# Kernel tuning notes

Hardware: AMD Instinct MI355X
Metric: run time of the kernel (lower is better)

The kernel has to match this reference:

```python
import jax, jax.numpy as jnp
import numpy as np

D_MODEL = 1024
NUM_EXP = 64
EPS = 1e-9
B, L = 16, 2048


def setup_inputs() -> dict:
    key = jax.random.key(0)
    ks = jax.random.split(key, 12)
    s = 1.0 / np.sqrt(D_MODEL)
    inp = {
        "x": jax.random.normal(ks[0], (B, L, D_MODEL), dtype=jnp.float32),
        "n_indexes": jax.random.randint(ks[1], (B, NUM_EXP), 0, NUM_EXP),
        "mask": jax.random.randint(ks[2], (B, 1, L), 0, 2).astype(jnp.int32),
        "q_emb": jax.random.normal(ks[3], (NUM_EXP, D_MODEL), dtype=jnp.float32),
        "b_emb": jax.random.normal(ks[4], (NUM_EXP, D_MODEL), dtype=jnp.float32),
        "Wk": jax.random.normal(ks[5], (D_MODEL, D_MODEL), dtype=jnp.float32) * s,
        "bk": jnp.zeros((D_MODEL,), jnp.float32),
        "Wa": jax.random.normal(ks[6], (D_MODEL, D_MODEL), dtype=jnp.float32) * s,
        "ba": jnp.zeros((D_MODEL,), jnp.float32),
        "Wb": jax.random.normal(ks[7], (D_MODEL, D_MODEL), dtype=jnp.float32) * s,
        "bb": jnp.zeros((D_MODEL,), jnp.float32),
        "Ws": jax.random.normal(ks[8], (D_MODEL, D_MODEL), dtype=jnp.float32) * s,
        "bs": jnp.zeros((D_MODEL,), jnp.float32),
    }
    return inp


def reference(x, n_indexes, mask, q_emb, b_emb, Wk, bk, Wa, ba, Wb, bb, Ws, bs):
    # Dropout layers act as identity (eval mode).
    query_exp = q_emb[n_indexes]          # [B, E, D]
    bias_exp = b_emb[n_indexes]           # [B, E, D]
    x_key = x @ Wk.T + bk                 # [B, L, D]
    z = jnp.einsum('bed,bld->bel', query_exp, x_key) / np.sqrt(D_MODEL)  # [B, E, L]

    maskf = (mask != 0).astype(z.dtype)   # broadcast [B,1,L]
    class_a_fw = jax.nn.relu(z) * maskf
    class_b_fw = jax.nn.relu(-z) * maskf
    class_a_fw = class_a_fw / (class_a_fw.sum(-1, keepdims=True) + EPS)
    class_b_fw = class_b_fw / (class_b_fw.sum(-1, keepdims=True) + EPS)

    class_a = jnp.einsum('bel,bld->bed', class_a_fw, x @ Wa.T + ba) + bias_exp
    class_b = jnp.einsum('bel,bld->bed', class_b_fw, x @ Wb.T + bb) + bias_exp

    zt = jnp.swapaxes(z, -2, -1)          # [B, L, E]  (unmasked, as in source)
    class_a_bw = jax.nn.relu(zt)
    class_b_bw = jax.nn.relu(-zt)
    class_a_bw = class_a_bw / (class_a_bw.sum(-1, keepdims=True) + EPS)
    class_b_bw = class_b_bw / (class_b_bw.sum(-1, keepdims=True) + EPS)

    class_a = jnp.einsum('ble,bed->bld', class_a_bw, class_a)  # [B, L, D]
    class_b = jnp.einsum('ble,bed->bld', class_b_bw, class_b)

    selector = jax.nn.sigmoid(x @ Ws.T + bs)
    return selector * class_a + (1.0 - selector) * class_b
```

## Files before the change

kernel.cpp:

```cpp
#include <hip/hip_runtime.h>
#include <math.h>

#define D_MODEL 1024
#define NUM_EXP 64
#define B_SZ 16
#define L_SZ 2048

using bf16x8  = __attribute__((ext_vector_type(8))) __bf16;
using floatx4 = __attribute__((ext_vector_type(4))) float;
using ushort8 = __attribute__((ext_vector_type(8))) unsigned short;
using ushort4v = __attribute__((ext_vector_type(4))) unsigned short;

__device__ __forceinline__ unsigned short f2bf(float f) {
    union { float f; unsigned u; } x; x.f = f;
    unsigned r = (x.u + 0x7fffu + ((x.u >> 16) & 1u)) >> 16;
    return (unsigned short)r;
}
__device__ __forceinline__ float bf2f(unsigned short h) {
    union { unsigned u; float f; } x; x.u = ((unsigned)h) << 16;
    return x.f;
}

#define GLD16(gp, lp) __builtin_amdgcn_global_load_lds( \
    (const __attribute__((address_space(1))) unsigned int*)(gp), \
    (__attribute__((address_space(3))) unsigned int*)(lp), 16, 0, 0)

__global__ void k_convx(const float* __restrict__ in, unsigned short* __restrict__ outN,
                        unsigned short* __restrict__ outT)
{
    __shared__ unsigned short T[64][65];
    const int b = blockIdx.z;
    const int l0 = blockIdx.y * 64, c0 = blockIdx.x * 64;
    const int t = threadIdx.x;
    const int tr = t >> 4, tc = (t & 15) * 4;
    const float* src = in + ((long)b * L_SZ + l0) * D_MODEL + c0;
    unsigned short* dN = outN + ((long)b * L_SZ + l0) * D_MODEL + c0;
    #pragma unroll
    for (int i = 0; i < 4; i++) {
        int r = tr + i * 16;
        float4 v = *(const float4*)(src + (long)r * D_MODEL + tc);
        ushort4v u; u[0]=f2bf(v.x); u[1]=f2bf(v.y); u[2]=f2bf(v.z); u[3]=f2bf(v.w);
        *(ushort4v*)(dN + (long)r * D_MODEL + tc) = u;
        T[r][tc+0]=u[0]; T[r][tc+1]=u[1]; T[r][tc+2]=u[2]; T[r][tc+3]=u[3];
    }
    __syncthreads();
    unsigned short* dT = outT + ((long)b * D_MODEL + c0) * L_SZ + l0;
    #pragma unroll
    for (int i = 0; i < 4; i++) {
        int c = tr + i * 16;
        ushort4v u;
        u[0]=T[tc+0][c]; u[1]=T[tc+1][c]; u[2]=T[tc+2][c]; u[3]=T[tc+3][c];
        *(ushort4v*)(dT + (long)c * L_SZ + tc) = u;
    }
}

__global__ void k_prep(const float* __restrict__ Wk,
                       const float* __restrict__ Wa, const float* __restrict__ Wb,
                       const float* __restrict__ Ws,
                       const int* __restrict__ idx, const float* __restrict__ q_emb,
                       const float* __restrict__ b_emb, const float* __restrict__ bk,
                       unsigned short* __restrict__ wkT,
                       unsigned short* __restrict__ oa, unsigned short* __restrict__ ob,
                       unsigned short* __restrict__ oc,
                       unsigned short* __restrict__ qexp, float* __restrict__ bias_exp,
                       float* __restrict__ qbk)
{
    __shared__ unsigned short T[64][65];
    __shared__ float red[4];
    const int blk = blockIdx.x;
    const int t = threadIdx.x;
    if (blk < 256) {
        const int r0 = (blk >> 4) * 64, c0 = (blk & 15) * 64;
        const int tr = t >> 4, tc = (t & 15) * 4;
        const float* src = Wk + (long)r0 * D_MODEL + c0;
        #pragma unroll
        for (int i = 0; i < 4; i++) {
            int r = tr + i * 16;
            float4 v = *(const float4*)(src + (long)r * D_MODEL + tc);
            T[r][tc+0]=f2bf(v.x); T[r][tc+1]=f2bf(v.y); T[r][tc+2]=f2bf(v.z); T[r][tc+3]=f2bf(v.w);
        }
        __syncthreads();
        unsigned short* dT = wkT + ((long)c0) * D_MODEL + r0;
        #pragma unroll
        for (int i = 0; i < 4; i++) {
            int c = tr + i * 16;
            ushort4v u;
            u[0]=T[tc+0][c]; u[1]=T[tc+1][c]; u[2]=T[tc+2][c]; u[3]=T[tc+3][c];
            *(ushort4v*)(dT + (long)c * D_MODEL + tc) = u;
        }
    } else if (blk < 256 + 1536) {
        long i = ((long)(blk - 256) * 256 + t) * 8;
        int which = (int)(i >> 20);
        long off = i & ((1L << 20) - 1);
        const float* src = which == 0 ? Wa : which == 1 ? Wb : Ws;
        unsigned short* dst = which == 0 ? oa : which == 1 ? ob : oc;
        float4 v0 = *(const float4*)(src + off);
        float4 v1 = *(const float4*)(src + off + 4);
        ushort8 r;
        r[0]=f2bf(v0.x); r[1]=f2bf(v0.y); r[2]=f2bf(v0.z); r[3]=f2bf(v0.w);
        r[4]=f2bf(v1.x); r[5]=f2bf(v1.y); r[6]=f2bf(v1.z); r[7]=f2bf(v1.w);
        *(ushort8*)(dst + off) = r;
    } else {
        const int be = blk - 1792;
        const int row = idx[be];
        const float* qs = q_emb + (long)row * D_MODEL;
        const float* bsrc = b_emb + (long)row * D_MODEL;
        float4 q4 = *(const float4*)(qs + t * 4);
        float4 k4 = *(const float4*)(bk + t * 4);
        float4 b4 = *(const float4*)(bsrc + t * 4);
        ushort4v r; r[0]=f2bf(q4.x); r[1]=f2bf(q4.y); r[2]=f2bf(q4.z); r[3]=f2bf(q4.w);
        *(ushort4v*)(qexp + (long)be * D_MODEL + t * 4) = r;
        *(float4*)(bias_exp + (long)be * D_MODEL + t * 4) = b4;
        float p = q4.x*k4.x + q4.y*k4.y + q4.z*k4.z + q4.w*k4.w;
        #pragma unroll
        for (int o = 32; o > 0; o >>= 1) p += __shfl_down(p, o);
        if ((t & 63) == 0) red[t >> 6] = p;
        __syncthreads();
        if (t == 0) qbk[be] = red[0] + red[1] + red[2] + red[3];
    }
}

__launch_bounds__(256)
__global__ void k_gemm_bt(const unsigned short* __restrict__ A,
                          const unsigned short* __restrict__ Bm,
                          const float* __restrict__ rowbias,
                          void* __restrict__ Cout,
                          int M, int N, int K, float scale, int flags,
                          long sA, long sB, long sC)
{
    __shared__ __align__(16) unsigned short As[64 * 32];
    __shared__ __align__(16) unsigned short Bs[64 * 32];
    const int bz = blockIdx.z;
    const unsigned short* Ab = A + (long)bz * sA;
    const unsigned short* Bb = Bm + (long)bz * sB;
    const int tid = threadIdx.x;
    const int wave = tid >> 6, lane = tid & 63;
    const int m0 = blockIdx.y * 64, n0 = blockIdx.x * 64;
    const int lrow = tid >> 2, lk = (tid & 3) * 8;
    const int q = lane >> 4, mr = lane & 15;

    floatx4 acc[4];
    floatx4 z4 = {0.f, 0.f, 0.f, 0.f};
    #pragma unroll
    for (int j = 0; j < 4; j++) acc[j] = z4;

    const unsigned short* Aptr = Ab + (long)(m0 + lrow) * K + lk;
    const unsigned short* Bptr = Bb + (long)(n0 + lrow) * K + lk;

    for (int k0 = 0; k0 < K; k0 += 32) {
        __syncthreads();
        *(ushort8*)&As[lrow * 32 + lk] = *(const ushort8*)(Aptr + k0);
        *(ushort8*)&Bs[lrow * 32 + lk] = *(const ushort8*)(Bptr + k0);
        __syncthreads();
        bf16x8 af = *(const bf16x8*)&As[(wave * 16 + mr) * 32 + q * 8];
        #pragma unroll
        for (int j = 0; j < 4; j++) {
            bf16x8 bfr = *(const bf16x8*)&Bs[(j * 16 + mr) * 32 + q * 8];
            acc[j] = __builtin_amdgcn_mfma_f32_16x16x32_bf16(af, bfr, acc[j], 0, 0, 0);
        }
    }
    #pragma unroll
    for (int j = 0; j < 4; j++) {
        int gn = n0 + j * 16 + mr;
        #pragma unroll
        for (int r = 0; r < 4; r++) {
            int gm = m0 + wave * 16 + q * 4 + r;
            float v = acc[j][r];
            if (rowbias) v += rowbias[(long)bz * M + gm];
            v *= scale;
            long cidx = (long)bz * sC + (long)gm * N + gn;
            if (flags & 1) ((unsigned short*)Cout)[cidx] = f2bf(v);
            else           ((float*)Cout)[cidx] = v;
        }
    }
}

__launch_bounds__(512)
__global__ void k_gemm_fw2(const unsigned short* __restrict__ A1,
                           const unsigned short* __restrict__ A2,
                           const unsigned short* __restrict__ Bt,
                           unsigned short* __restrict__ C1,
                           unsigned short* __restrict__ C2)
{
    __shared__ __align__(16) unsigned short As1[2][64 * 32];
    __shared__ __align__(16) unsigned short As2[2][64 * 32];
    __shared__ __align__(16) unsigned short Bs[2][64 * 32];
    __shared__ float Red[2][64][65];
    const int bz = blockIdx.z;
    const int n0 = blockIdx.x * 64;
    const int tid = threadIdx.x;
    const int grp = tid >> 8;
    const int gtid = tid & 255;
    const int wave = gtid >> 6, lane = tid & 63;
    const int lrow = gtid >> 2, lk = (gtid & 3) * 8;
    const int q = lane >> 4, mr = lane & 15;
    const int kb = grp * (L_SZ / 2);

    const unsigned short* a1p = A1 + ((long)bz * NUM_EXP + lrow) * L_SZ + kb + lk;
    const unsigned short* a2p = A2 + ((long)bz * NUM_EXP + lrow) * L_SZ + kb + lk;
    const unsigned short* bp  = Bt + ((long)bz * D_MODEL + n0 + lrow) * L_SZ + kb + lk;

    floatx4 acc1[4], acc2[4];
    floatx4 z4 = {0.f, 0.f, 0.f, 0.f};
    #pragma unroll
    for (int j = 0; j < 4; j++) { acc1[j] = z4; acc2[j] = z4; }

    for (int k0 = 0; k0 < L_SZ / 2; k0 += 32) {
        __syncthreads();
        *(ushort8*)&As1[grp][lrow * 32 + lk] = *(const ushort8*)(a1p + k0);
        *(ushort8*)&As2[grp][lrow * 32 + lk] = *(const ushort8*)(a2p + k0);
        *(ushort8*)&Bs[grp][lrow * 32 + lk]  = *(const ushort8*)(bp + k0);
        __syncthreads();
        bf16x8 f1 = *(const bf16x8*)&As1[grp][(wave * 16 + mr) * 32 + q * 8];
        bf16x8 f2 = *(const bf16x8*)&As2[grp][(wave * 16 + mr) * 32 + q * 8];
        #pragma unroll
        for (int j = 0; j < 4; j++) {
            bf16x8 bb = *(const bf16x8*)&Bs[grp][(j * 16 + mr) * 32 + q * 8];
            acc1[j] = __builtin_amdgcn_mfma_f32_16x16x32_bf16(f1, bb, acc1[j], 0, 0, 0);
            acc2[j] = __builtin_amdgcn_mfma_f32_16x16x32_bf16(f2, bb, acc2[j], 0, 0, 0);
        }
    }
    __syncthreads();
    if (grp == 1) {
        #pragma unroll
        for (int j = 0; j < 4; j++)
            #pragma unroll
            for (int r = 0; r < 4; r++) {
                int gm = wave * 16 + q * 4 + r;
                Red[0][gm][j * 16 + mr] = acc1[j][r];
                Red[1][gm][j * 16 + mr] = acc2[j][r];
            }
    }
    __syncthreads();
    if (grp == 0) {
        #pragma unroll
        for (int j = 0; j < 4; j++) {
            int gn = n0 + j * 16 + mr;
            #pragma unroll
            for (int r = 0; r < 4; r++) {
                int gm = wave * 16 + q * 4 + r;
                long cidx = ((long)bz * NUM_EXP + gm) * D_MODEL + gn;
                C1[cidx] = f2bf(acc1[j][r] + Red[0][gm][j * 16 + mr]);
                C2[cidx] = f2bf(acc2[j][r] + Red[1][gm][j * 16 + mr]);
            }
        }
    }
}

__launch_bounds__(256)
__global__ void k_gemm_cls(const unsigned short* __restrict__ fwxA, const unsigned short* __restrict__ fwxB,
                           const unsigned short* __restrict__ Wa_, const unsigned short* __restrict__ Wb_,
                           const float* __restrict__ ba_, const float* __restrict__ bb_,
                           const float* __restrict__ wsA, const float* __restrict__ wsB,
                           const float* __restrict__ biasE,
                           unsigned short* __restrict__ aHi, unsigned short* __restrict__ aLo,
                           unsigned short* __restrict__ bHi, unsigned short* __restrict__ bLo)
{
    __shared__ __align__(16) unsigned short As[64 * 32];
    __shared__ __align__(16) unsigned short Bs[64 * 32];
    const int zz = blockIdx.z;
    const int side = zz >> 4, bz = zz & 15;
    const unsigned short* Ab = (side ? fwxB : fwxA) + (long)bz * NUM_EXP * D_MODEL;
    const unsigned short* Bb = side ? Wb_ : Wa_;
    const float* cb = side ? bb_ : ba_;
    const float* rw = (side ? wsB : wsA) + bz * NUM_EXP;
    const float* bE = biasE + (long)bz * NUM_EXP * D_MODEL;
    unsigned short* oHi = (side ? bHi : aHi) + (long)bz * NUM_EXP * D_MODEL;
    unsigned short* oLo = (side ? bLo : aLo) + (long)bz * NUM_EXP * D_MODEL;

    const int tid = threadIdx.x;
    const int wave = tid >> 6, lane = tid & 63;
    const int n0 = blockIdx.x * 64;
    const int lrow = tid >> 2, lk = (tid & 3) * 8;
    const int q = lane >> 4, mr = lane & 15;

    floatx4 acc[4];
    floatx4 z4 = {0.f, 0.f, 0.f, 0.f};
    #pragma unroll
    for (int j = 0; j < 4; j++) acc[j] = z4;

    const unsigned short* Aptr = Ab + (long)lrow * D_MODEL + lk;
    const unsigned short* Bptr = Bb + (long)(n0 + lrow) * D_MODEL + lk;

    for (int k0 = 0; k0 < D_MODEL; k0 += 32) {
        __syncthreads();
        *(ushort8*)&As[lrow * 32 + lk] = *(const ushort8*)(Aptr + k0);
        *(ushort8*)&Bs[lrow * 32 + lk] = *(const ushort8*)(Bptr + k0);
        __syncthreads();
        bf16x8 af = *(const bf16x8*)&As[(wave * 16 + mr) * 32 + q * 8];
        #pragma unroll
        for (int j = 0; j < 4; j++) {
            bf16x8 bfr = *(const bf16x8*)&Bs[(j * 16 + mr) * 32 + q * 8];
            acc[j] = __builtin_amdgcn_mfma_f32_16x16x32_bf16(af, bfr, acc[j], 0, 0, 0);
        }
    }
    #pragma unroll
    for (int j = 0; j < 4; j++) {
        int gn = n0 + j * 16 + mr;
        float cbv = cb[gn];
        #pragma unroll
        for (int r = 0; r < 4; r++) {
            int gm = wave * 16 + q * 4 + r;
            float v = acc[j][r] + rw[gm] * cbv + bE[(long)gm * D_MODEL + gn];
            unsigned short hi = f2bf(v);
            long tix = (long)gn * NUM_EXP + gm;
            oHi[tix] = hi;
            oLo[tix] = f2bf(v - bf2f(hi));
        }
    }
}

__launch_bounds__(512, 2)
__global__ void k_gemm_sel(const unsigned short* __restrict__ A,
                           const unsigned short* __restrict__ Bm,
                           const float* __restrict__ bias,
                           unsigned short* __restrict__ C)
{
    __shared__ __align__(16) unsigned short As[2][2][8192];
    __shared__ __align__(16) unsigned short Bs[2][2][8192];

    const int tid = threadIdx.x;
    const int wid = tid >> 6, lane = tid & 63;
    const int q = lane >> 4, mr = lane & 15;
    const int wm = wid >> 2, wn = wid & 3;
    const int kread = (q ^ ((mr >> 1) & 3)) * 8;

    const int bid = blockIdx.x;
    const int wg = (bid & 7) * 32 + (bid >> 3);
    const int m0 = (wg >> 1) * 256;
    const int npair = wg & 1;

    const unsigned short* Ag = A + (long)m0 * 1024;
    const unsigned short* Bg0 = Bm + (long)(npair * 512) * 1024;
    const unsigned short* Bg1 = Bg0 + (long)256 * 1024;

    const int srow = tid >> 2;
    const int sgrp = (tid & 3) ^ ((srow >> 1) & 3);
    const long soff = (long)srow * 1024 + sgrp * 8;
    const int ldst = wid * 64 * 8;

    auto STAGE = [&](int g) {
        int T = g >> 2; if (T > 31) T = 31;
        const int kh = (g >> 1) & 1, isB = g & 1;
        const int tl = T & 15;
        const unsigned short* base = isB ? (T < 16 ? Bg0 : Bg1) : Ag;
        const unsigned short* src = base + (long)tl * 64 + kh * 32 + soff;
        unsigned short* dst = (isB ? &Bs[0][0][0] : &As[0][0][0])
                              + ((tl & 1) * 2 + kh) * 8192 + ldst;
        GLD16(src, dst);
        GLD16(src + 128 * 1024, dst + 4096);
    };

    floatx4 acc[8][4];
    floatx4 z4 = {0.f, 0.f, 0.f, 0.f};
    #pragma unroll
    for (int i = 0; i < 8; i++)
        #pragma unroll
        for (int j = 0; j < 4; j++) acc[i][j] = z4;

    STAGE(0); STAGE(1); STAGE(2); STAGE(3); STAGE(4); STAGE(5);
    asm volatile("s_waitcnt vmcnt(4)" ::: "memory");
    __builtin_amdgcn_s_barrier();

    for (int h = 0; h < 2; h++) {
        for (int t = 0; t < 16; t++) {
            const unsigned short* Abuf = &As[t & 1][0][0];
            const unsigned short* Bbuf = &Bs[t & 1][0][0];
            bf16x8 bfr[4];
            #pragma unroll
            for (int p = 0; p < 4; p++) {
                const int kh = p >> 1, mh = p & 1;
                bf16x8 af[4];
                #pragma unroll
                for (int i = 0; i < 4; i++)
                    af[i] = *(const bf16x8*)&Abuf[kh * 8192 +
                            (wm * 128 + mh * 64 + i * 16 + mr) * 32 + kread];
                if (mh == 0) {
                    #pragma unroll
                    for (int j = 0; j < 4; j++)
                        bfr[j] = *(const bf16x8*)&Bbuf[kh * 8192 +
                                 (wn * 64 + j * 16 + mr) * 32 + kread];
                }
                STAGE(h * 64 + 4 * t + p + 6);
                if (mh == 1) asm volatile("s_waitcnt vmcnt(8)" ::: "memory");
                __builtin_amdgcn_s_barrier();
                asm volatile("s_waitcnt lgkmcnt(0)" ::: "memory");
                __builtin_amdgcn_sched_barrier(0);
                __builtin_amdgcn_s_setprio(1);
                #pragma unroll
                for (int i = 0; i < 4; i++)
                    #pragma unroll
                    for (int j = 0; j < 4; j++)
                        acc[mh * 4 + i][j] = __builtin_amdgcn_mfma_f32_16x16x32_bf16(
                            af[i], bfr[j], acc[mh * 4 + i][j], 0, 0, 0);
                __builtin_amdgcn_s_setprio(0);
                __builtin_amdgcn_s_barrier();
                __builtin_amdgcn_sched_barrier(0);
            }
        }
        const int n0 = npair * 512 + h * 256;
        #pragma unroll
        for (int i = 0; i < 8; i++) {
            #pragma unroll
            for (int j = 0; j < 4; j++) {
                const int gn = n0 + wn * 64 + j * 16 + mr;
                const float cbv = bias[gn];
                #pragma unroll
                for (int r = 0; r < 4; r++) {
                    const int gm = m0 + wm * 128 + i * 16 + q * 4 + r;
                    C[(long)gm * 1024 + gn] = f2bf(acc[i][j][r] + cbv);
                    if (h == 0) acc[i][j][r] = 0.f;
                }
            }
        }
    }
    asm volatile("s_waitcnt vmcnt(0)" ::: "memory");
}

__global__ void k_norms(const float* __restrict__ z, const int* __restrict__ mask,
                        unsigned short* __restrict__ a_fw, unsigned short* __restrict__ b_fw,
                        float* __restrict__ wsum_a, float* __restrict__ wsum_b,
                        unsigned short* __restrict__ a_bw, unsigned short* __restrict__ b_bw)
{
    const int blk = blockIdx.x;
    const int tid = threadIdx.x;
    if (blk < 1024) {
        const int be = blk;
        const int b = be >> 6;
        const float* zr = z + (long)be * L_SZ;
        const int* mr = mask + (long)b * L_SZ;
        float sa = 0.f, sb = 0.f;
        for (int l = tid; l < L_SZ; l += 256) {
            float v = zr[l];
            if (mr[l] != 0) { sa += fmaxf(v, 0.f); sb += fmaxf(-v, 0.f); }
        }
        #pragma unroll
        for (int o = 32; o > 0; o >>= 1) { sa += __shfl_down(sa, o); sb += __shfl_down(sb, o); }
        __shared__ float red[8];
        int wave = tid >> 6, lane = tid & 63;
        if (lane == 0) { red[wave] = sa; red[4 + wave] = sb; }
        __syncthreads();
        float ta = red[0] + red[1] + red[2] + red[3];
        float tb = red[4] + red[5] + red[6] + red[7];
        float ia = 1.f / (ta + 1e-9f), ib = 1.f / (tb + 1e-9f);
        if (tid == 0) { wsum_a[be] = ta * ia; wsum_b[be] = tb * ib; }
        for (int l = tid; l < L_SZ; l += 256) {
            float v = zr[l];
            float m = (mr[l] != 0) ? 1.f : 0.f;
            a_fw[(long)be * L_SZ + l] = f2bf(fmaxf(v, 0.f) * m * ia);
            b_fw[(long)be * L_SZ + l] = f2bf(fmaxf(-v, 0.f) * m * ib);
        }
    } else {
        int r = (blk - 1024) * 256 + tid;
        int b = r >> 11, l = r & 2047;
        const float* zb = z + (long)b * NUM_EXP * L_SZ + l;
        float sa = 0.f, sb = 0.f;
        float va[NUM_EXP];
        #pragma unroll 8
        for (int e = 0; e < NUM_EXP; e++) {
            float v = zb[(long)e * L_SZ];
            va[e] = v;
            sa += fmaxf(v, 0.f); sb += fmaxf(-v, 0.f);
        }
        float ia = 1.f / (sa + 1e-9f), ib = 1.f / (sb + 1e-9f);
        unsigned short* ar = a_bw + (long)r * NUM_EXP;
        unsigned short* br = b_bw + (long)r * NUM_EXP;
        #pragma unroll 8
        for (int e = 0; e < NUM_EXP; e++) {
            float v = va[e];
            ar[e] = f2bf(fmaxf(v, 0.f) * ia);
            br[e] = f2bf(fmaxf(-v, 0.f) * ib);
        }
    }
}

__launch_bounds__(256)
__global__ void k_final_mfma(const unsigned short* __restrict__ aw,
                             const unsigned short* __restrict__ bw,
                             const unsigned short* __restrict__ caHi,
                             const unsigned short* __restrict__ caLo,
                             const unsigned short* __restrict__ cbHi,
                             const unsigned short* __restrict__ cbLo,
                             const unsigned short* __restrict__ selbf,
                             float* __restrict__ out)
{
    __shared__ __align__(16) unsigned short Aa[64 * 72];
    __shared__ __align__(16) unsigned short Ab[64 * 72];
    __shared__ __align__(16) unsigned short BaH[64 * 72];
    __shared__ __align__(16) unsigned short BaL[64 * 72];
    __shared__ __align__(16) unsigned short BbH[64 * 72];
    __shared__ __align__(16) unsigned short BbL[64 * 72];
    const int bz = blockIdx.z;
    const int l0 = blockIdx.y * 64, d0 = blockIdx.x * 64;
    const int tid = threadIdx.x;
    const int wave = tid >> 6, lane = tid & 63;
    const int q = lane >> 4, mr = lane & 15;

    const unsigned short* awb = aw + ((long)bz * L_SZ + l0) * NUM_EXP;
    const unsigned short* bwb = bw + ((long)bz * L_SZ + l0) * NUM_EXP;
    const long cbase = ((long)bz * D_MODEL + d0) * NUM_EXP;

    #pragma unroll
    for (int c = 0; c < 2; c++) {
        int idx = c * 256 + tid;
        int row = idx >> 3, kc = (idx & 7) * 8;
        int lw = row * 72 + kc;
        long ga = (long)row * NUM_EXP + kc;
        *(ushort8*)&Aa[lw]  = *(const ushort8*)(awb + ga);
        *(ushort8*)&Ab[lw]  = *(const ushort8*)(bwb + ga);
        *(ushort8*)&BaH[lw] = *(const ushort8*)(caHi + cbase + ga);
        *(ushort8*)&BaL[lw] = *(const ushort8*)(caLo + cbase + ga);
        *(ushort8*)&BbH[lw] = *(const ushort8*)(cbHi + cbase + ga);
        *(ushort8*)&BbL[lw] = *(const ushort8*)(cbLo + cbase + ga);
    }
    __syncthreads();

    floatx4 accA[4], accB[4];
    floatx4 z4 = {0.f, 0.f, 0.f, 0.f};
    #pragma unroll
    for (int j = 0; j < 4; j++) { accA[j] = z4; accB[j] = z4; }

    #pragma unroll
    for (int ks = 0; ks < 2; ks++) {
        int ko = ks * 32 + q * 8;
        bf16x8 fa = *(const bf16x8*)&Aa[(wave * 16 + mr) * 72 + ko];
        bf16x8 fb = *(const bf16x8*)&Ab[(wave * 16 + mr) * 72 + ko];
        #pragma unroll
        for (int j = 0; j < 4; j++) {
            int bo = (j * 16 + mr) * 72 + ko;
            accA[j] = __builtin_amdgcn_mfma_f32_16x16x32_bf16(fa, *(const bf16x8*)&BaH[bo], accA[j], 0, 0, 0);
            accA[j] = __builtin_amdgcn_mfma_f32_16x16x32_bf16(fa, *(const bf16x8*)&BaL[bo], accA[j], 0, 0, 0);
            accB[j] = __builtin_amdgcn_mfma_f32_16x16x32_bf16(fb, *(const bf16x8*)&BbH[bo], accB[j], 0, 0, 0);
            accB[j] = __builtin_amdgcn_mfma_f32_16x16x32_bf16(fb, *(const bf16x8*)&BbL[bo], accB[j], 0, 0, 0);
        }
    }

    #pragma unroll
    for (int j = 0; j < 4; j++) {
        #pragma unroll
        for (int r = 0; r < 4; r++) {
            int gl = l0 + wave * 16 + q * 4 + r;
            int gd = d0 + j * 16 + mr;
            long o = ((long)bz * L_SZ + gl) * D_MODEL + gd;
            float s = 1.f / (1.f + __expf(-bf2f(selbf[o])));
            out[o] = s * accA[j][r] + (1.f - s) * accB[j][r];
        }
    }
}

extern "C" void kernel_launch(void* const* d_in, const int* in_sizes, int n_in,
                              void* d_out, int out_size, void* d_ws, size_t ws_size,
                              hipStream_t stream)
{
    const float* x     = (const float*)d_in[0];
    const int*   nidx  = (const int*)d_in[1];
    const int*   mask  = (const int*)d_in[2];
    const float* q_emb = (const float*)d_in[3];
    const float* b_emb = (const float*)d_in[4];
    const float* Wk    = (const float*)d_in[5];
    const float* bk    = (const float*)d_in[6];
    const float* Wa    = (const float*)d_in[7];
    const float* ba    = (const float*)d_in[8];
    const float* Wb    = (const float*)d_in[9];
    const float* bb    = (const float*)d_in[10];
    const float* Ws    = (const float*)d_in[11];
    const float* bs    = (const float*)d_in[12];
    float* out = (float*)d_out;

    constexpr long BLD = (long)B_SZ * L_SZ * D_MODEL;
    constexpr long BEL = (long)B_SZ * NUM_EXP * L_SZ;
    constexpr long BED = (long)B_SZ * NUM_EXP * D_MODEL;
    constexpr long DD  = (long)D_MODEL * D_MODEL;

    char* w = (char*)d_ws;
    size_t off = 0;
    auto carve = [&](size_t bytes) { char* p = w + off; off += (bytes + 255) & ~(size_t)255; return p; };
    unsigned short* x_bf   = (unsigned short*)carve(BLD * 2);
    unsigned short* x_bfT  = (unsigned short*)carve(BLD * 2);
    unsigned short* wkT_bf = (unsigned short*)carve(DD * 2);
    unsigned short* wa_bf  = (unsigned short*)carve(DD * 2);
    unsigned short* wb_bf  = (unsigned short*)carve(DD * 2);
    unsigned short* ws_bf  = (unsigned short*)carve(DD * 2);
    unsigned short* qexp   = (unsigned short*)carve(BED * 2);
    float*          bias_e = (float*)carve(BED * 4);
    float*          qbk    = (float*)carve(B_SZ * NUM_EXP * 4);
    unsigned short* qk     = (unsigned short*)carve(BED * 2);
    float*          z      = (float*)carve(BEL * 4);
    unsigned short* a_fw   = (unsigned short*)carve(BEL * 2);
    unsigned short* b_fw   = (unsigned short*)carve(BEL * 2);
    float*          wsum_a = (float*)carve(B_SZ * NUM_EXP * 4);
    float*          wsum_b = (float*)carve(B_SZ * NUM_EXP * 4);
    unsigned short* a_bw   = (unsigned short*)carve(BEL * 2);
    unsigned short* b_bw   = (unsigned short*)carve(BEL * 2);
    unsigned short* fwx_a  = (unsigned short*)carve(BED * 2);
    unsigned short* fwx_b  = (unsigned short*)carve(BED * 2);
    unsigned short* caHi   = (unsigned short*)carve(BED * 2);
    unsigned short* caLo   = (unsigned short*)carve(BED * 2);
    unsigned short* cbHi   = (unsigned short*)carve(BED * 2);
    unsigned short* cbLo   = (unsigned short*)carve(BED * 2);
    if (ws_size < off) return;
    unsigned short* selbf = x_bfT;

    k_convx<<<dim3(16, 32, B_SZ), 256, 0, stream>>>(x, x_bf, x_bfT);
    k_prep<<<2816, 256, 0, stream>>>(Wk, Wa, Wb, Ws, nidx, q_emb, b_emb, bk,
                                     wkT_bf, wa_bf, wb_bf, ws_bf, qexp, bias_e, qbk);

    k_gemm_bt<<<dim3(16, 1, B_SZ), 256, 0, stream>>>(qexp, wkT_bf, nullptr, qk,
        NUM_EXP, D_MODEL, D_MODEL, 1.f, 1, (long)NUM_EXP * D_MODEL, 0, (long)NUM_EXP * D_MODEL);

    k_gemm_bt<<<dim3(32, 1, B_SZ), 256, 0, stream>>>(qk, x_bf, qbk, z,
        NUM_EXP, L_SZ, D_MODEL, 1.f / 32.f, 0,
        (long)NUM_EXP * D_MODEL, (long)L_SZ * D_MODEL, (long)NUM_EXP * L_SZ);

    k_norms<<<1152, 256, 0, stream>>>(z, mask, a_fw, b_fw, wsum_a, wsum_b, a_bw, b_bw);

    k_gemm_fw2<<<dim3(16, 1, B_SZ), 512, 0, stream>>>(a_fw, b_fw, x_bfT, fwx_a, fwx_b);

    k_gemm_sel<<<256, 512, 0, stream>>>(x_bf, ws_bf, bs, selbf);

    k_gemm_cls<<<dim3(16, 1, 32), 256, 0, stream>>>(fwx_a, fwx_b, wa_bf, wb_bf, ba, bb,
        wsum_a, wsum_b, bias_e, caHi, caLo, cbHi, cbLo);

    k_final_mfma<<<dim3(16, 32, B_SZ), 256, 0, stream>>>(a_bw, b_bw, caHi, caLo, cbHi, cbLo, selbf, out);
}
```

Before: 523.6 us.

## Split-K small GEMMs, fuse backward norm into z GEMM, retile selector GEMM

Measured after the change: 506.8 us. -3.2%, faster.

```diff
diff --git a/kernel.cpp b/kernel.cpp
--- a/kernel.cpp
+++ b/kernel.cpp
@@ -120,57 +120,149 @@
     }
 }
 
-__launch_bounds__(256)
-__global__ void k_gemm_bt(const unsigned short* __restrict__ A,
-                          const unsigned short* __restrict__ Bm,
-                          const float* __restrict__ rowbias,
-                          void* __restrict__ Cout,
-                          int M, int N, int K, float scale, int flags,
-                          long sA, long sB, long sC)
-{
-    __shared__ __align__(16) unsigned short As[64 * 32];
-    __shared__ __align__(16) unsigned short Bs[64 * 32];
-    const int bz = blockIdx.z;
-    const unsigned short* Ab = A + (long)bz * sA;
-    const unsigned short* Bb = Bm + (long)bz * sB;
+__launch_bounds__(512)
+__global__ void k_gemm_qk64(const unsigned short* __restrict__ qexp,
+                            const unsigned short* __restrict__ WkT,
+                            unsigned short* __restrict__ Cq)
+{
+    __shared__ __align__(16) unsigned short As[2][64 * 32];
+    __shared__ __align__(16) unsigned short Bs2[2][64 * 32];
+    __shared__ float Red[64][65];
+    const int bz = blockIdx.z, n0 = blockIdx.x * 64;
     const int tid = threadIdx.x;
-    const int wave = tid >> 6, lane = tid & 63;
-    const int m0 = blockIdx.y * 64, n0 = blockIdx.x * 64;
-    const int lrow = tid >> 2, lk = (tid & 3) * 8;
+    const int grp = tid >> 8, gtid = tid & 255;
+    const int wave = gtid >> 6, lane = tid & 63;
+    const int lrow = gtid >> 2, lk = (gtid & 3) * 8;
     const int q = lane >> 4, mr = lane & 15;
+    const int kb = grp * (D_MODEL / 2);
+
+    const unsigned short* Ap = qexp + ((long)bz * NUM_EXP + lrow) * D_MODEL + kb + lk;
+    const unsigned short* Bp = WkT + (long)(n0 + lrow) * D_MODEL + kb + lk;
 
     floatx4 acc[4];
     floatx4 z4 = {0.f, 0.f, 0.f, 0.f};
     #pragma unroll
     for (int j = 0; j < 4; j++) acc[j] = z4;
 
-    const unsigned short* Aptr = Ab + (long)(m0 + lrow) * K + lk;
-    const unsigned short* Bptr = Bb + (long)(n0 + lrow) * K + lk;
-
-    for (int k0 = 0; k0 < K; k0 += 32) {
-        __syncthreads();
-        *(ushort8*)&As[lrow * 32 + lk] = *(const ushort8*)(Aptr + k0);
-        *(ushort8*)&Bs[lrow * 32 + lk] = *(const ushort8*)(Bptr + k0);
-        __syncthreads();
-        bf16x8 af = *(const bf16x8*)&As[(wave * 16 + mr) * 32 + q * 8];
-        #pragma unroll
-        for (int j = 0; j < 4; j++) {
-            bf16x8 bfr = *(const bf16x8*)&Bs[(j * 16 + mr) * 32 + q * 8];
+    for (int k0 = 0; k0 < D_MODEL / 2; k0 += 32) {
+        __syncthreads();
+        *(ushort8*)&As[grp][lrow * 32 + lk] = *(const ushort8*)(Ap + k0);
+        *(ushort8*)&Bs2[grp][lrow * 32 + lk] = *(const ushort8*)(Bp + k0);
+        __syncthreads();
+        bf16x8 af = *(const bf16x8*)&As[grp][(wave * 16 + mr) * 32 + q * 8];
+        #pragma unroll
+        for (int j = 0; j < 4; j++) {
+            bf16x8 bfr = *(const bf16x8*)&Bs2[grp][(j * 16 + mr) * 32 + q * 8];
             acc[j] = __builtin_amdgcn_mfma_f32_16x16x32_bf16(af, bfr, acc[j], 0, 0, 0);
         }
     }
-    #pragma unroll
-    for (int j = 0; j < 4; j++) {
-        int gn = n0 + j * 16 + mr;
-        #pragma unroll
-        for (int r = 0; r < 4; r++) {
-            int gm = m0 + wave * 16 + q * 4 + r;
-            float v = acc[j][r];
-            if (rowbias) v += rowbias[(long)bz * M + gm];
-            v *= scale;
-            long cidx = (long)bz * sC + (long)gm * N + gn;
-            if (flags & 1) ((unsigned short*)Cout)[cidx] = f2bf(v);
-            else           ((float*)Cout)[cidx] = v;
+    __syncthreads();
+    if (grp == 1) {
+        #pragma unroll
+        for (int j = 0; j < 4; j++)
+            #pragma unroll
+            for (int r = 0; r < 4; r++)
+                Red[wave * 16 + q * 4 + r][j * 16 + mr] = acc[j][r];
+    }
+    __syncthreads();
+    if (grp == 0) {
+        #pragma unroll
+        for (int j = 0; j < 4; j++) {
+            int gn = n0 + j * 16 + mr;
+            #pragma unroll
+            for (int r = 0; r < 4; r++) {
+                int gm = wave * 16 + q * 4 + r;
+                Cq[((long)bz * NUM_EXP + gm) * D_MODEL + gn] =
+                    f2bf(acc[j][r] + Red[gm][j * 16 + mr]);
+            }
+        }
+    }
+}
+
+__launch_bounds__(512)
+__global__ void k_gemm_z(const unsigned short* __restrict__ qk,
+                         const unsigned short* __restrict__ x_bf,
+                         const float* __restrict__ qbk,
+                         float* __restrict__ z,
+                         unsigned short* __restrict__ a_bw,
+                         unsigned short* __restrict__ b_bw)
+{
+    __shared__ __align__(16) unsigned short As[2][64 * 32];
+    __shared__ __align__(16) unsigned short Bs2[2][64 * 32];
+    __shared__ float Red[64][65];
+    const int bz = blockIdx.z, n0 = blockIdx.x * 64;
+    const int tid = threadIdx.x;
+    const int grp = tid >> 8, gtid = tid & 255;
+    const int wave = gtid >> 6, lane = tid & 63;
+    const int lrow = gtid >> 2, lk = (gtid & 3) * 8;
+    const int q = lane >> 4, mr = lane & 15;
+    const int kb = grp * (D_MODEL / 2);
+
+    const unsigned short* Ap = qk + ((long)bz * NUM_EXP + lrow) * D_MODEL + kb + lk;
+    const unsigned short* Bp = x_bf + ((long)bz * L_SZ + n0 + lrow) * D_MODEL + kb + lk;
+
+    floatx4 acc[4];
+    floatx4 z4 = {0.f, 0.f, 0.f, 0.f};
+    #pragma unroll
+    for (int j = 0; j < 4; j++) acc[j] = z4;
+
+    for (int k0 = 0; k0 < D_MODEL / 2; k0 += 32) {
+        __syncthreads();
+        *(ushort8*)&As[grp][lrow * 32 + lk] = *(const ushort8*)(Ap + k0);
+        *(ushort8*)&Bs2[grp][lrow * 32 + lk] = *(const ushort8*)(Bp + k0);
+        __syncthreads();
+        bf16x8 af = *(const bf16x8*)&As[grp][(wave * 16 + mr) * 32 + q * 8];
+        #pragma unroll
+        for (int j = 0; j < 4; j++) {
+            bf16x8 bfr = *(const bf16x8*)&Bs2[grp][(j * 16 + mr) * 32 + q * 8];
+            acc[j] = __builtin_amdgcn_mfma_f32_16x16x32_bf16(af, bfr, acc[j], 0, 0, 0);
+        }
+    }
+    __syncthreads();
+    if (grp == 1) {
+        #pragma unroll
+        for (int j = 0; j < 4; j++)
+            #pragma unroll
+            for (int r = 0; r < 4; r++)
+                Red[wave * 16 + q * 4 + r][j * 16 + mr] = acc[j][r];
+    }
+    __syncthreads();
+    if (grp == 0) {
+        #pragma unroll
+        for (int j = 0; j < 4; j++) {
+            int gn = n0 + j * 16 + mr;
+            #pragma unroll
+            for (int r = 0; r < 4; r++) {
+                int gm = wave * 16 + q * 4 + r;
+                float v = (acc[j][r] + Red[gm][j * 16 + mr] + qbk[bz * NUM_EXP + gm]) * (1.f / 32.f);
+                z[((long)bz * NUM_EXP + gm) * L_SZ + gn] = v;
+                Red[gm][j * 16 + mr] = v;
+            }
+        }
+    }
+    __syncthreads();
+    if (tid < 64) {
+        const int l = n0 + tid;
+        float sa = 0.f, sb = 0.f;
+        #pragma unroll
+        for (int e = 0; e < NUM_EXP; e++) {
+            float v = Red[e][tid];
+            sa += fmaxf(v, 0.f); sb += fmaxf(-v, 0.f);
+        }
+        float ia = 1.f / (sa + 1e-9f), ib = 1.f / (sb + 1e-9f);
+        unsigned short* ar = a_bw + ((long)bz * L_SZ + l) * NUM_EXP;
+        unsigned short* br = b_bw + ((long)bz * L_SZ + l) * NUM_EXP;
+        #pragma unroll
+        for (int eo = 0; eo < NUM_EXP; eo += 8) {
+            ushort8 ra, rb;
+            #pragma unroll
+            for (int k = 0; k < 8; k++) {
+                float v = Red[eo + k][tid];
+                ra[k] = f2bf(fmaxf(v, 0.f) * ia);
+                rb[k] = f2bf(fmaxf(-v, 0.f) * ib);
+            }
+            *(ushort8*)(ar + eo) = ra;
+            *(ushort8*)(br + eo) = rb;
         }
     }
 }
@@ -247,17 +339,18 @@
     }
 }
 
-__launch_bounds__(256)
-__global__ void k_gemm_cls(const unsigned short* __restrict__ fwxA, const unsigned short* __restrict__ fwxB,
-                           const unsigned short* __restrict__ Wa_, const unsigned short* __restrict__ Wb_,
-                           const float* __restrict__ ba_, const float* __restrict__ bb_,
-                           const float* __restrict__ wsA, const float* __restrict__ wsB,
-                           const float* __restrict__ biasE,
-                           unsigned short* __restrict__ aHi, unsigned short* __restrict__ aLo,
-                           unsigned short* __restrict__ bHi, unsigned short* __restrict__ bLo)
-{
-    __shared__ __align__(16) unsigned short As[64 * 32];
-    __shared__ __align__(16) unsigned short Bs[64 * 32];
+__launch_bounds__(512)
+__global__ void k_gemm_cls64(const unsigned short* __restrict__ fwxA, const unsigned short* __restrict__ fwxB,
+                             const unsigned short* __restrict__ Wa_, const unsigned short* __restrict__ Wb_,
+                             const float* __restrict__ ba_, const float* __restrict__ bb_,
+                             const float* __restrict__ wsA, const float* __restrict__ wsB,
+                             const float* __restrict__ biasE,
+                             unsigned short* __restrict__ aHi, unsigned short* __restrict__ aLo,
+                             unsigned short* __restrict__ bHi, unsigned short* __restrict__ bLo)
+{
+    __shared__ __align__(16) unsigned short As[2][64 * 32];
+    __shared__ __align__(16) unsigned short Bs2[2][64 * 32];
+    __shared__ float Red[64][65];
     const int zz = blockIdx.z;
     const int side = zz >> 4, bz = zz & 15;
     const unsigned short* Ab = (side ? fwxB : fwxA) + (long)bz * NUM_EXP * D_MODEL;
@@ -269,43 +362,57 @@
     unsigned short* oLo = (side ? bLo : aLo) + (long)bz * NUM_EXP * D_MODEL;
 
     const int tid = threadIdx.x;
-    const int wave = tid >> 6, lane = tid & 63;
+    const int grp = tid >> 8, gtid = tid & 255;
+    const int wave = gtid >> 6, lane = tid & 63;
     const int n0 = blockIdx.x * 64;
-    const int lrow = tid >> 2, lk = (tid & 3) * 8;
+    const int lrow = gtid >> 2, lk = (gtid & 3) * 8;
     const int q = lane >> 4, mr = lane & 15;
+    const int kb = grp * (D_MODEL / 2);
 
     floatx4 acc[4];
     floatx4 z4 = {0.f, 0.f, 0.f, 0.f};
     #pragma unroll
     for (int j = 0; j < 4; j++) acc[j] = z4;
 
-    const unsigned short* Aptr = Ab + (long)lrow * D_MODEL + lk;
-    const unsigned short* Bptr = Bb + (long)(n0 + lrow) * D_MODEL + lk;
-
-    for (int k0 = 0; k0 < D_MODEL; k0 += 32) {
-        __syncthreads();
-        *(ushort8*)&As[lrow * 32 + lk] = *(const ushort8*)(Aptr + k0);
-        *(ushort8*)&Bs[lrow * 32 + lk] = *(const ushort8*)(Bptr + k0);
-        __syncthreads();
-        bf16x8 af = *(const bf16x8*)&As[(wave * 16 + mr) * 32 + q * 8];
-        #pragma unroll
-        for (int j = 0; j < 4; j++) {
-            bf16x8 bfr = *(const bf16x8*)&Bs[(j * 16 + mr) * 32 + q * 8];
+    const unsigned short* Aptr = Ab + (long)lrow * D_MODEL + kb + lk;
+    const unsigned short* Bptr = Bb + (long)(n0 + lrow) * D_MODEL + kb + lk;
+
+    for (int k0 = 0; k0 < D_MODEL / 2; k0 += 32) {
+        __syncthreads();
+        *(ushort8*)&As[grp][lrow * 32 + lk] = *(const ushort8*)(Aptr + k0);
+        *(ushort8*)&Bs2[grp][lrow * 32 + lk] = *(const ushort8*)(Bptr + k0);
+        __syncthreads();
+        bf16x8 af = *(const bf16x8*)&As[grp][(wave * 16 + mr) * 32 + q * 8];
+        #pragma unroll
+        for (int j = 0; j < 4; j++) {
+            bf16x8 bfr = *(const bf16x8*)&Bs2[grp][(j * 16 + mr) * 32 + q * 8];
             acc[j] = __builtin_amdgcn_mfma_f32_16x16x32_bf16(af, bfr, acc[j], 0, 0, 0);
         }
     }
-    #pragma unroll
-    for (int j = 0; j < 4; j++) {
-        int gn = n0 + j * 16 + mr;
-        float cbv = cb[gn];
-        #pragma unroll
-        for (int r = 0; r < 4; r++) {
-            int gm = wave * 16 + q * 4 + r;
-            float v = acc[j][r] + rw[gm] * cbv + bE[(long)gm * D_MODEL + gn];
-            unsigned short hi = f2bf(v);
-            long tix = (long)gn * NUM_EXP + gm;
-            oHi[tix] = hi;
-            oLo[tix] = f2bf(v - bf2f(hi));
+    __syncthreads();
+    if (grp == 1) {
+        #pragma unroll
+        for (int j = 0; j < 4; j++)
+            #pragma unroll
+            for (int r = 0; r < 4; r++)
+                Red[wave * 16 + q * 4 + r][j * 16 + mr] = acc[j][r];
+    }
+    __syncthreads();
+    if (grp == 0) {
+        #pragma unroll
+        for (int j = 0; j < 4; j++) {
+            int gn = n0 + j * 16 + mr;
+            float cbv = cb[gn];
+            #pragma unroll
+            for (int r = 0; r < 4; r++) {
+                int gm = wave * 16 + q * 4 + r;
+                float v = acc[j][r] + Red[gm][j * 16 + mr] + rw[gm] * cbv
+                          + bE[(long)gm * D_MODEL + gn];
+                unsigned short hi = f2bf(v);
+                long tix = (long)gn * NUM_EXP + gm;
+                oHi[tix] = hi;
+                oLo[tix] = f2bf(v - bf2f(hi));
+            }
         }
     }
 }
@@ -326,13 +433,12 @@
     const int kread = (q ^ ((mr >> 1) & 3)) * 8;
 
     const int bid = blockIdx.x;
-    const int wg = (bid & 7) * 32 + (bid >> 3);
-    const int m0 = (wg >> 1) * 256;
-    const int npair = wg & 1;
+    const int wg = (bid & 7) * 64 + (bid >> 3);
+    const int m0 = (wg >> 2) * 256;
+    const int n0 = (wg & 3) * 256;
 
     const unsigned short* Ag = A + (long)m0 * 1024;
-    const unsigned short* Bg0 = Bm + (long)(npair * 512) * 1024;
-    const unsigned short* Bg1 = Bg0 + (long)256 * 1024;
+    const unsigned short* Bg = Bm + (long)n0 * 1024;
 
     const int srow = tid >> 2;
     const int sgrp = (tid & 3) ^ ((srow >> 1) & 3);
@@ -340,13 +446,11 @@
     const int ldst = wid * 64 * 8;
 
     auto STAGE = [&](int g) {
-        int T = g >> 2; if (T > 31) T = 31;
+        int tile = g >> 2; if (tile > 15) tile = 15;
         const int kh = (g >> 1) & 1, isB = g & 1;
-        const int tl = T & 15;
-        const unsigned short* base = isB ? (T < 16 ? Bg0 : Bg1) : Ag;
-        const unsigned short* src = base + (long)tl * 64 + kh * 32 + soff;
+        const unsigned short* src = (isB ? Bg : Ag) + (long)tile * 64 + kh * 32 + soff;
         unsigned short* dst = (isB ? &Bs[0][0][0] : &As[0][0][0])
-                              + ((tl & 1) * 2 + kh) * 8192 + ldst;
+                              + ((tile & 1) * 2 + kh) * 8192 + ldst;
         GLD16(src, dst);
         GLD16(src + 128 * 1024, dst + 4096);
     };
@@ -362,115 +466,87 @@
     asm volatile("s_waitcnt vmcnt(4)" ::: "memory");
     __builtin_amdgcn_s_barrier();
 
-    for (int h = 0; h < 2; h++) {
-        for (int t = 0; t < 16; t++) {
-            const unsigned short* Abuf = &As[t & 1][0][0];
-            const unsigned short* Bbuf = &Bs[t & 1][0][0];
-            bf16x8 bfr[4];
-            #pragma unroll
-            for (int p = 0; p < 4; p++) {
-                const int kh = p >> 1, mh = p & 1;
-                bf16x8 af[4];
+    for (int t = 0; t < 16; t++) {
+        const unsigned short* Abuf = &As[t & 1][0][0];
+        const unsigned short* Bbuf = &Bs[t & 1][0][0];
+        bf16x8 bfr[4];
+        #pragma unroll
+        for (int p = 0; p < 4; p++) {
+            const int kh = p >> 1, mh = p & 1;
+            bf16x8 af[4];
+            #pragma unroll
+            for (int i = 0; i < 4; i++)
+                af[i] = *(const bf16x8*)&Abuf[kh * 8192 +
+                        (wm * 128 + mh * 64 + i * 16 + mr) * 32 + kread];
+            if (mh == 0) {
                 #pragma unroll
-                for (int i = 0; i < 4; i++)
-                    af[i] = *(const bf16x8*)&Abuf[kh * 8192 +
-                            (wm * 128 + mh * 64 + i * 16 + mr) * 32 + kread];
-                if (mh == 0) {
-                    #pragma unroll
-                    for (int j = 0; j < 4; j++)
-                        bfr[j] = *(const bf16x8*)&Bbuf[kh * 8192 +
-                                 (wn * 64 + j * 16 + mr) * 32 + kread];
-                }
-                STAGE(h * 64 + 4 * t + p + 6);
-                if (mh == 1) asm volatile("s_waitcnt vmcnt(8)" ::: "memory");
-                __builtin_amdgcn_s_barrier();
-                asm volatile("s_waitcnt lgkmcnt(0)" ::: "memory");
-                __builtin_amdgcn_sched_barrier(0);
-                __builtin_amdgcn_s_setprio(1);
+                for (int j = 0; j < 4; j++)
+                    bfr[j] = *(const bf16x8*)&Bbuf[kh * 8192 +
+                             (wn * 64 + j * 16 + mr) * 32 + kread];
+            }
+            STAGE(4 * t + p + 6);
+            if (mh == 1) asm volatile("s_waitcnt vmcnt(8)" ::: "memory");
+            __builtin_amdgcn_s_barrier();
+            asm volatile("s_waitcnt lgkmcnt(0)" ::: "memory");
+            __builtin_amdgcn_sched_barrier(0);
+            __builtin_amdgcn_s_setprio(1);
+            #pragma unroll
+            for (int i = 0; i < 4; i++)
                 #pragma unroll
-                for (int i = 0; i < 4; i++)
-                    #pragma unroll
-                    for (int j = 0; j < 4; j++)
-                        acc[mh * 4 + i][j] = __builtin_amdgcn_mfma_f32_16x16x32_bf16(
-                            af[i], bfr[j], acc[mh * 4 + i][j], 0, 0, 0);
-                __builtin_amdgcn_s_setprio(0);
-                __builtin_amdgcn_s_barrier();
-                __builtin_amdgcn_sched_barrier(0);
-            }
-        }
-        const int n0 = npair * 512 + h * 256;
-        #pragma unroll
-        for (int i = 0; i < 8; i++) {
-            #pragma unroll
-            for (int j = 0; j < 4; j++) {
-                const int gn = n0 + wn * 64 + j * 16 + mr;
-                const float cbv = bias[gn];
-                #pragma unroll
-                for (int r = 0; r < 4; r++) {
-                    const int gm = m0 + wm * 128 + i * 16 + q * 4 + r;
-                    C[(long)gm * 1024 + gn] = f2bf(acc[i][j][r] + cbv);
-                    if (h == 0) acc[i][j][r] = 0.f;
-                }
-            }
+                for (int j = 0; j < 4; j++)
+                    acc[mh * 4 + i][j] = __builtin_amdgcn_mfma_f32_16x16x32_bf16(
+                        af[i], bfr[j], acc[mh * 4 + i][j], 0, 0, 0);
+            __builtin_amdgcn_s_setprio(0);
+            __builtin_amdgcn_s_barrier();
+            __builtin_amdgcn_sched_barrier(0);
         }
     }
     asm volatile("s_waitcnt vmcnt(0)" ::: "memory");
-}
-
-__global__ void k_norms(const float* __restrict__ z, const int* __restrict__ mask,
-                        unsigned short* __restrict__ a_fw, unsigned short* __restrict__ b_fw,
-                        float* __restrict__ wsum_a, float* __restrict__ wsum_b,
-                        unsigned short* __restrict__ a_bw, unsigned short* __restrict__ b_bw)
-{
-    const int blk = blockIdx.x;
+
+    #pragma unroll
+    for (int i = 0; i < 8; i++) {
+        #pragma unroll
+        for (int j = 0; j < 4; j++) {
+            const int gn = n0 + wn * 64 + j * 16 + mr;
+            const float cbv = bias[gn];
+            #pragma unroll
+            for (int r = 0; r < 4; r++) {
+                const int gm = m0 + wm * 128 + i * 16 + q * 4 + r;
+                C[(long)gm * 1024 + gn] = f2bf(acc[i][j][r] + cbv);
+            }
+        }
+    }
+}
+
+__global__ void k_fwnorm(const float* __restrict__ z, const int* __restrict__ mask,
+                         unsigned short* __restrict__ a_fw, unsigned short* __restrict__ b_fw,
+                         float* __restrict__ wsum_a, float* __restrict__ wsum_b)
+{
+    const int be = blockIdx.x;
+    const int b = be >> 6;
+    const float* zr = z + (long)be * L_SZ;
+    const int* mr = mask + (long)b * L_SZ;
     const int tid = threadIdx.x;
-    if (blk < 1024) {
-        const int be = blk;
-        const int b = be >> 6;
-        const float* zr = z + (long)be * L_SZ;
-        const int* mr = mask + (long)b * L_SZ;
-        float sa = 0.f, sb = 0.f;
-        for (int l = tid; l < L_SZ; l += 256) {
-            float v = zr[l];
-            if (mr[l] != 0) { sa += fmaxf(v, 0.f); sb += fmaxf(-v, 0.f); }
-        }
-        #pragma unroll
-        for (int o = 32; o > 0; o >>= 1) { sa += __shfl_down(sa, o); sb += __shfl_down(sb, o); }
-        __shared__ float red[8];
-        int wave = tid >> 6, lane = tid & 63;
-        if (lane == 0) { red[wave] = sa; red[4 + wave] = sb; }
-        __syncthreads();
-        float ta = red[0] + red[1] + red[2] + red[3];
-        float tb = red[4] + red[5] + red[6] + red[7];
-        float ia = 1.f / (ta + 1e-9f), ib = 1.f / (tb + 1e-9f);
-        if (tid == 0) { wsum_a[be] = ta * ia; wsum_b[be] = tb * ib; }
-        for (int l = tid; l < L_SZ; l += 256) {
-            float v = zr[l];
-            float m = (mr[l] != 0) ? 1.f : 0.f;
-            a_fw[(long)be * L_SZ + l] = f2bf(fmaxf(v, 0.f) * m * ia);
-            b_fw[(long)be * L_SZ + l] = f2bf(fmaxf(-v, 0.f) * m * ib);
-        }
-    } else {
-        int r = (blk - 1024) * 256 + tid;
-        int b = r >> 11, l = r & 2047;
-        const float* zb = z + (long)b * NUM_EXP * L_SZ + l;
-        float sa = 0.f, sb = 0.f;
-        float va[NUM_EXP];
-        #pragma unroll 8
-        for (int e = 0; e < NUM_EXP; e++) {
-            float v = zb[(long)e * L_SZ];
-            va[e] = v;
-            sa += fmaxf(v, 0.f); sb += fmaxf(-v, 0.f);
-        }
-        float ia = 1.f / (sa + 1e-9f), ib = 1.f / (sb + 1e-9f);
-        unsigned short* ar = a_bw + (long)r * NUM_EXP;
-        unsigned short* br = b_bw + (long)r * NUM_EXP;
-        #pragma unroll 8
-        for (int e = 0; e < NUM_EXP; e++) {
-            float v = va[e];
-            ar[e] = f2bf(fmaxf(v, 0.f) * ia);
-            br[e] = f2bf(fmaxf(-v, 0.f) * ib);
-        }
+    float sa = 0.f, sb = 0.f;
+    for (int l = tid; l < L_SZ; l += 256) {
+        float v = zr[l];
+        if (mr[l] != 0) { sa += fmaxf(v, 0.f); sb += fmaxf(-v, 0.f); }
+    }
+    #pragma unroll
+    for (int o = 32; o > 0; o >>= 1) { sa += __shfl_down(sa, o); sb += __shfl_down(sb, o); }
+    __shared__ float red[8];
+    int wave = tid >> 6, lane = tid & 63;
+    if (lane == 0) { red[wave] = sa; red[4 + wave] = sb; }
+    __syncthreads();
+    float ta = red[0] + red[1] + red[2] + red[3];
+    float tb = red[4] + red[5] + red[6] + red[7];
+    float ia = 1.f / (ta + 1e-9f), ib = 1.f / (tb + 1e-9f);
+    if (tid == 0) { wsum_a[be] = ta * ia; wsum_b[be] = tb * ib; }
+    for (int l = tid; l < L_SZ; l += 256) {
+        float v = zr[l];
+        float m = (mr[l] != 0) ? 1.f : 0.f;
+        a_fw[(long)be * L_SZ + l] = f2bf(fmaxf(v, 0.f) * m * ia);
+        b_fw[(long)be * L_SZ + l] = f2bf(fmaxf(-v, 0.f) * m * ib);
     }
 }
 
@@ -605,20 +681,17 @@
     k_prep<<<2816, 256, 0, stream>>>(Wk, Wa, Wb, Ws, nidx, q_emb, b_emb, bk,
                                      wkT_bf, wa_bf, wb_bf, ws_bf, qexp, bias_e, qbk);
 
-    k_gemm_bt<<<dim3(16, 1, B_SZ), 256, 0, stream>>>(qexp, wkT_bf, nullptr, qk,
-        NUM_EXP, D_MODEL, D_MODEL, 1.f, 1, (long)NUM_EXP * D_MODEL, 0, (long)NUM_EXP * D_MODEL);
-
-    k_gemm_bt<<<dim3(32, 1, B_SZ), 256, 0, stream>>>(qk, x_bf, qbk, z,
-        NUM_EXP, L_SZ, D_MODEL, 1.f / 32.f, 0,
-        (long)NUM_EXP * D_MODEL, (long)L_SZ * D_MODEL, (long)NUM_EXP * L_SZ);
-
-    k_norms<<<1152, 256, 0, stream>>>(z, mask, a_fw, b_fw, wsum_a, wsum_b, a_bw, b_bw);
+    k_gemm_qk64<<<dim3(16, 1, B_SZ), 512, 0, stream>>>(qexp, wkT_bf, qk);
+
+    k_gemm_z<<<dim3(32, 1, B_SZ), 512, 0, stream>>>(qk, x_bf, qbk, z, a_bw, b_bw);
+
+    k_fwnorm<<<B_SZ * NUM_EXP, 256, 0, stream>>>(z, mask, a_fw, b_fw, wsum_a, wsum_b);
 
     k_gemm_fw2<<<dim3(16, 1, B_SZ), 512, 0, stream>>>(a_fw, b_fw, x_bfT, fwx_a, fwx_b);
 
-    k_gemm_sel<<<256, 512, 0, stream>>>(x_bf, ws_bf, bs, selbf);
-
-    k_gemm_cls<<<dim3(16, 1, 32), 256, 0, stream>>>(fwx_a, fwx_b, wa_bf, wb_bf, ba, bb,
+    k_gemm_sel<<<512, 512, 0, stream>>>(x_bf, ws_bf, bs, selbf);
+
+    k_gemm_cls64<<<dim3(16, 1, 32), 512, 0, stream>>>(fwx_a, fwx_b, wa_bf, wb_bf, ba, bb,
         wsum_a, wsum_b, bias_e, caHi, caLo, cbHi, cbLo);
 
     k_final_mfma<<<dim3(16, 32, B_SZ), 256, 0, stream>>>(a_bw, b_bw, caHi, caLo, cbHi, cbLo, selbf, out);
```
